# Optimization experiments

Hardware: AMD Instinct MI355X
Metric: run time of the kernel (lower is better)

Reference implementation:

```python
import jax, jax.numpy as jnp
import numpy as np

H, D, E, N, F = 16, 128, 2048, 2048, 8192
EPS = 1e-5


def setup_inputs() -> dict:
    key = jax.random.key(0)
    ks = jax.random.split(key, 11)
    u = lambda k, s: jax.random.uniform(k, s, dtype=jnp.float32)  # torch.rand init
    return {
        "token_embeddings": jax.random.normal(ks[0], (N, E), dtype=jnp.float32),
        "W_Q": u(ks[1], (H, E, D)),
        "W_K": u(ks[2], (H, E, D)),
        "W_V": u(ks[3], (H, E, D)),
        "W_Pool": u(ks[4], (H * D, E)),
        "W_1": u(ks[5], (E, F)),
        "b_1": u(ks[6], (1, F)),
        "W_2": u(ks[7], (F, E)),
        "b_2": u(ks[8], (1, E)),
        "gamma": u(ks[9], (1, 1)),
        "beta": u(ks[10], (1, E)),
    }


def _layer_norm(x, gamma, beta):
    mean = jnp.mean(x, axis=-1, keepdims=True)
    var = jnp.var(x, axis=-1, keepdims=True)  # unbiased=False
    return gamma * (x - mean) * jax.lax.rsqrt(var + EPS) + beta


def _mha(x, W_Q, W_K, W_V, W_Pool):
    # Q,K,V: [H, N, D]
    Q = jnp.einsum("ne,hed->hnd", x, W_Q)
    K = jnp.einsum("ne,hed->hnd", x, W_K)
    V = jnp.einsum("ne,hed->hnd", x, W_V)
    scores = jnp.einsum("hnd,hmd->hnm", Q, K) / jnp.sqrt(jnp.float32(D))
    causal = jnp.tril(jnp.ones((N, N), dtype=bool))
    scores = jnp.where(causal, scores, -jnp.inf)
    attn = jax.nn.softmax(scores, axis=-1)  # [H, N, N]
    heads = jnp.einsum("hnm,hmd->hnd", attn, V)  # [H, N, D]
    concat = jnp.transpose(heads, (1, 0, 2)).reshape(N, H * D)
    return concat @ W_Pool


def reference(token_embeddings, W_Q, W_K, W_V, W_Pool, W_1, b_1, W_2, b_2, gamma, beta):
    x = token_embeddings
    x = x + _mha(x, W_Q, W_K, W_V, W_Pool)
    x = _layer_norm(x, gamma, beta)
    ffn = jax.nn.relu(x @ W_1 + b_1) @ W_2 + b_2
    x = x + ffn
    x = _layer_norm(x, gamma, beta)
    return x
```

## Files before the change

kernel.cpp:

```cpp
#include <hip/hip_runtime.h>

typedef unsigned short u16;
typedef unsigned int   u32;
typedef __attribute__((ext_vector_type(4))) float f32x4;
typedef __attribute__((ext_vector_type(8))) short bf16x8;

#define MFMA_B16(a,b,c) __builtin_amdgcn_mfma_f32_16x16x32_bf16((a),(b),(c),0,0,0)

__device__ __forceinline__ u16 f2bf(float f){
  u32 u = __builtin_bit_cast(u32, f);
  u32 r = (u + 0x7FFFu + ((u >> 16) & 1u)) >> 16;
  return (u16)r;
}
__device__ __forceinline__ float bf2f(u16 h){
  u32 u = ((u32)h) << 16;
  return __builtin_bit_cast(float, u);
}
__device__ __forceinline__ void gload16(const void* g, void* l){
  __builtin_amdgcn_global_load_lds((const __attribute__((address_space(1))) void*)g,
                                   (__attribute__((address_space(3))) void*)l, 16, 0, 0);
}

__global__ __launch_bounds__(256) void pack_x2(const float* __restrict__ x,
                                               u16* __restrict__ xh, u16* __restrict__ xl){
  const int i = blockIdx.x*256 + threadIdx.x;
  const float v = x[i];
  const u16 hi = f2bf(v);
  xh[i] = hi;
  xl[i] = f2bf(v - bf2f(hi));
}

__global__ __launch_bounds__(256) void pack_qkv2(const float* __restrict__ WQ, const float* __restrict__ WK,
                                                 const float* __restrict__ WV,
                                                 u16* __restrict__ outh, u16* __restrict__ outl){
  __shared__ float t32[32][33];
  const int tid = threadIdx.x;
  const int tx = tid & 31, ty = tid >> 5;
  const int et = blockIdx.x >> 2, dt = blockIdx.x & 3;
  const int hh = blockIdx.y, tt = blockIdx.z;
  const float* W = (tt == 0 ? WQ : (tt == 1 ? WK : WV)) + (size_t)hh*2048*128;
  #pragma unroll
  for (int i = 0; i < 4; i++)
    t32[ty + i*8][tx] = W[(size_t)(et*32 + ty + i*8)*128 + dt*32 + tx];
  __syncthreads();
  const int j0 = tt*2048 + hh*128 + dt*32;
  #pragma unroll
  for (int i = 0; i < 4; i++){
    const float v = t32[tx][ty + i*8];
    const u16 hi = f2bf(v);
    const u16 lo = f2bf(v - bf2f(hi));
    const size_t idx = (size_t)(j0 + ty + i*8)*2048 + (et*32 + tx);
    outh[idx] = hi; outl[idx] = lo;
  }
}

__global__ __launch_bounds__(256) void tpack2(const float* __restrict__ in,
                                              u16* __restrict__ outh, u16* __restrict__ outl,
                                              int R, int C){
  __shared__ float t32[32][33];
  const int tid = threadIdx.x;
  const int tx = tid & 31, ty = tid >> 5;
  const int c0 = blockIdx.x*32, r0 = blockIdx.y*32;
  #pragma unroll
  for (int i = 0; i < 4; i++)
    t32[ty + i*8][tx] = in[(size_t)(r0 + ty + i*8)*C + c0 + tx];
  __syncthreads();
  #pragma unroll
  for (int i = 0; i < 4; i++){
    const float v = t32[tx][ty + i*8];
    const u16 hi = f2bf(v);
    const u16 lo = f2bf(v - bf2f(hi));
    const size_t idx = (size_t)(c0 + ty + i*8)*R + r0 + tx;
    outh[idx] = hi; outl[idx] = lo;
  }
}

template<int NS, int EPI, int SK>
__global__ __launch_bounds__(512, 2) void gemm8(
    const u16* __restrict__ Ah, const u16* __restrict__ Al,
    const u16* __restrict__ Bh, const u16* __restrict__ Bl,
    float* __restrict__ outf, u16* __restrict__ outb,
    const float* __restrict__ bias,
    u16* __restrict__ qh, u16* __restrict__ ql,
    u16* __restrict__ kh, u16* __restrict__ kl,
    u16* __restrict__ vTh, float* __restrict__ part,
    int M, int N, int K)
{
  __shared__ u16 LS[2][2][16384];
  const int tid = threadIdx.x;
  const int lane = tid & 63;
  const int w = tid >> 6;
  const int wr = w >> 2, wc = w & 3;
  const int l15 = lane & 15, lh = lane >> 4;
  const int nbx = N >> 8;
  int bsw = ((int)blockIdx.x & 7) * ((int)gridDim.x >> 3) + ((int)blockIdx.x >> 3);
  int slice = 0;
  if (SK == 4){ slice = bsw & 3; bsw >>= 2; }
  const int bx = bsw % nbx, by = bsw / nbx;
  const int m0 = by << 8, n0 = bx << 8;

  const int tiles_total = (NS * K) >> 6;
  const int nt = (SK == 4) ? (tiles_total >> 2) : tiles_total;
  const int t0 = (SK == 4) ? slice * nt : 0;

  auto stage = [&](int buf, int t){
    const int k0v = t << 6;
    const u16* Ap; const u16* Bp; int kk;
    if (NS == 1){ Ap = Ah; Bp = Bh; kk = k0v; }
    else if (NS == 2){
      if (k0v < K){ Ap = Ah; Bp = Bh; kk = k0v; }
      else        { Ap = Ah; Bp = Bl; kk = k0v - K; }
    } else {
      if (k0v < K)        { Ap = Ah; Bp = Bh; kk = k0v; }
      else if (k0v < 2*K) { Ap = Ah; Bp = Bl; kk = k0v - K; }
      else                { Ap = Al; Bp = Bh; kk = k0v - 2*K; }
    }
    u16* La = &LS[buf][0][0];
    u16* Lb = &LS[buf][1][0];
    #pragma unroll
    for (int q = 0; q < 4; q++){
      int s = q*512 + tid;
      int row = s >> 3, cc = (s & 7) ^ (row & 7);
      gload16(Ap + (size_t)(m0+row)*K + kk + cc*8, La + (q*512 + (tid & 448))*8);
    }
    #pragma unroll
    for (int q = 0; q < 4; q++){
      int s = q*512 + tid;
      int row = s >> 3, cc = (s & 7) ^ (row & 7);
      gload16(Bp + (size_t)(n0+row)*K + kk + cc*8, Lb + (q*512 + (tid & 448))*8);
    }
  };

  f32x4 acc[8][4] = {};
  bf16x8 bfr[4][2];

  stage(0, t0);
  for (int lt = 0; lt < nt; ++lt){
    const int buf = lt & 1;
    if (lt + 1 < nt){
      stage(buf ^ 1, t0 + lt + 1);
      asm volatile("s_waitcnt vmcnt(8)" ::: "memory");
    } else {
      asm volatile("s_waitcnt vmcnt(0)" ::: "memory");
    }
    asm volatile("" ::: "memory");
    __builtin_amdgcn_s_barrier();
    asm volatile("" ::: "memory");

    const u16* La = &LS[buf][0][0];
    const u16* Lb = &LS[buf][1][0];
    #pragma unroll
    for (int n = 0; n < 4; n++){
      int br = wc*64 + n*16 + l15;
      #pragma unroll
      for (int kt = 0; kt < 2; kt++){
        int c = (kt*4 + lh) ^ (br & 7);
        bfr[n][kt] = *(const bf16x8*)(Lb + br*64 + c*8);
      }
    }
    #pragma unroll
    for (int p = 0; p < 4; p++){
      if (p){
        asm volatile("" ::: "memory");
        __builtin_amdgcn_s_barrier();
        asm volatile("" ::: "memory");
      }
      bf16x8 af[2][2];
      #pragma unroll
      for (int i = 0; i < 2; i++){
        int ar = wr*128 + (2*p+i)*16 + l15;
        #pragma unroll
        for (int kt = 0; kt < 2; kt++){
          int c = (kt*4 + lh) ^ (ar & 7);
          af[i][kt] = *(const bf16x8*)(La + ar*64 + c*8);
        }
      }
      asm volatile("s_waitcnt lgkmcnt(0)" ::: "memory");
      __builtin_amdgcn_sched_barrier(0);
      __builtin_amdgcn_s_setprio(1);
      #pragma unroll
      for (int i = 0; i < 2; i++)
        #pragma unroll
        for (int n = 0; n < 4; n++)
          #pragma unroll
          for (int kt = 0; kt < 2; kt++)
            acc[2*p+i][n] = MFMA_B16(af[i][kt], bfr[n][kt], acc[2*p+i][n]);
      __builtin_amdgcn_s_setprio(0);
    }
    asm volatile("" ::: "memory");
    __builtin_amdgcn_s_barrier();
    asm volatile("" ::: "memory");
  }

  #pragma unroll
  for (int m = 0; m < 8; m++){
    #pragma unroll
    for (int n = 0; n < 4; n++){
      const int rbase = m0 + wr*128 + m*16 + lh*4;
      const int col = n0 + wc*64 + n*16 + l15;
      if (EPI == 0){
        const int plane = col >> 11;
        const int cj = col & 2047;
        if (plane == 2){
          ushort4 h4 = make_ushort4(f2bf(acc[m][n][0]), f2bf(acc[m][n][1]),
                                    f2bf(acc[m][n][2]), f2bf(acc[m][n][3]));
          *(ushort4*)(vTh + (size_t)cj*2048 + rbase) = h4;
        } else {
          u16* hp = (plane == 0) ? qh : kh;
          u16* lp = (plane == 0) ? ql : kl;
          #pragma unroll
          for (int r = 0; r < 4; r++){
            float v = acc[m][n][r];
            u16 hi = f2bf(v);
            u16 lo = f2bf(v - bf2f(hi));
            hp[(size_t)(rbase+r)*2048 + cj] = hi;
            lp[(size_t)(rbase+r)*2048 + cj] = lo;
          }
        }
      } else if (EPI == 2){
        const float b = bias[col];
        #pragma unroll
        for (int r = 0; r < 4; r++){
          float v = acc[m][n][r] + b;
          outb[(size_t)(rbase+r)*N + col] = f2bf(v > 0.f ? v : 0.f);
        }
      } else {
        float* dst = (slice < 3) ? (part + (size_t)slice*M*N) : outf;
        #pragma unroll
        for (int r = 0; r < 4; r++)
          dst[(size_t)(rbase+r)*N + col] = acc[m][n][r];
      }
    }
  }
}

__global__ __launch_bounds__(256) void ffn2_reduce(
    float* __restrict__ PR, const float* __restrict__ part,
    const float* __restrict__ H1, const float* __restrict__ b2)
{
  const size_t i4 = (size_t)blockIdx.x*256 + threadIdx.x;
  const size_t base = i4*4;
  const int col = (int)(base & 2047);
  float4 a  = ((float4*)PR)[i4];
  float4 p0 = ((const float4*)part)[i4];
  float4 p1 = ((const float4*)(part + 4194304))[i4];
  float4 p2 = ((const float4*)(part + 8388608))[i4];
  float4 h  = ((const float4*)H1)[i4];
  float4 b  = *(const float4*)(b2 + col);
  a.x = a.x + p0.x + p1.x + p2.x + h.x + b.x;
  a.y = a.y + p0.y + p1.y + p2.y + h.y + b.y;
  a.z = a.z + p0.z + p1.z + p2.z + h.z + b.z;
  a.w = a.w + p0.w + p1.w + p2.w + h.w + b.w;
  ((float4*)PR)[i4] = a;
}

__global__ __launch_bounds__(256) void gemm_bt(
    const u16* __restrict__ Ah, const u16* __restrict__ Bh,
    float* __restrict__ outf, const float* __restrict__ res,
    int M, int N, int K)
{
  __shared__ u16 As[2][128*64];
  __shared__ u16 Bs[2][128*64];
  const int tid = threadIdx.x;
  const int lane = tid & 63;
  const int w = tid >> 6;
  const int l15 = lane & 15, lh = lane >> 4;
  const int nbx = N >> 7;
  const int bsw = ((int)blockIdx.x & 7)*((int)gridDim.x >> 3) + ((int)blockIdx.x >> 3);
  const int bx = bsw % nbx, by = bsw / nbx;
  const int m0 = by << 7, n0 = bx << 7;
  const int wm = (w >> 1) << 6, wn = (w & 1) << 6;

  f32x4 acc[4][4] = {};
  const int NT = K >> 6;

  auto stage = [&](int buf, int kk){
    u16* Asb = &As[buf][0];
    u16* Bsb = &Bs[buf][0];
    #pragma unroll
    for (int q = 0; q < 4; q++){
      int s = q*256 + tid;
      int row = s >> 3, cc = (s & 7) ^ (row & 7);
      gload16(Ah + (size_t)(m0+row)*K + kk + cc*8, Asb + (q*256 + (tid & 192))*8);
    }
    #pragma unroll
    for (int q = 0; q < 4; q++){
      int s = q*256 + tid;
      int row = s >> 3, cc = (s & 7) ^ (row & 7);
      gload16(Bh + (size_t)(n0+row)*K + kk + cc*8, Bsb + (q*256 + (tid & 192))*8);
    }
  };

  stage(0, 0);
  for (int t = 0; t < NT; ++t){
    const int cur = t & 1;
    if (t + 1 < NT){
      stage(cur ^ 1, (t + 1) << 6);
      asm volatile("s_waitcnt vmcnt(8)" ::: "memory");
    } else {
      asm volatile("s_waitcnt vmcnt(0)" ::: "memory");
    }
    __builtin_amdgcn_s_barrier();
    asm volatile("" ::: "memory");

    const u16* Asb = &As[cur][0];
    const u16* Bsb = &Bs[cur][0];
    #pragma unroll
    for (int kt = 0; kt < 2; kt++){
      bf16x8 af[4], bfr[4];
      #pragma unroll
      for (int m = 0; m < 4; m++){
        int row = wm + m*16 + l15;
        int c = (kt*4 + lh) ^ (row & 7);
        af[m] = *(const bf16x8*)(Asb + row*64 + c*8);
      }
      #pragma unroll
      for (int n = 0; n < 4; n++){
        int row = wn + n*16 + l15;
        int c = (kt*4 + lh) ^ (row & 7);
        bfr[n] = *(const bf16x8*)(Bsb + row*64 + c*8);
      }
      #pragma unroll
      for (int m = 0; m < 4; m++)
        #pragma unroll
        for (int n = 0; n < 4; n++)
          acc[m][n] = MFMA_B16(af[m], bfr[n], acc[m][n]);
    }
    asm volatile("" ::: "memory");
    __builtin_amdgcn_s_barrier();
    asm volatile("" ::: "memory");
  }

  #pragma unroll
  for (int m = 0; m < 4; m++){
    #pragma unroll
    for (int n = 0; n < 4; n++){
      const int rbase = m0 + wm + m*16 + lh*4;
      const int col = n0 + wn + n*16 + l15;
      #pragma unroll
      for (int r = 0; r < 4; r++){
        size_t idx = (size_t)(rbase+r)*N + col;
        outf[idx] = acc[m][n][r] + res[idx];
      }
    }
  }
}

__global__ __launch_bounds__(256) void attn_k(
    const u16* __restrict__ qh, const u16* __restrict__ ql,
    const u16* __restrict__ kh, const u16* __restrict__ kl,
    const u16* __restrict__ vT, u16* __restrict__ atth)
{
  __shared__ u16 Khs[64*128];
  __shared__ u16 Kls[64*128];
  __shared__ u16 Vhs[128*64];
  __shared__ u16 Phs[4*16*64];

  const int tid = threadIdx.x;
  const int lane = tid & 63;
  const int w = tid >> 6;
  const int l15 = lane & 15, lh = lane >> 4;
  const int h = blockIdx.y;
  const int qb = blockIdx.x;
  const int qbase = qb << 6;
  const float scale = 0.088388347648318447f;

  bf16x8 qfh[4], qfl[4];
  {
    const int qrow = qbase + w*16 + l15;
    const u16* ph = qh + (size_t)qrow*2048 + h*128 + lh*8;
    const u16* pl = ql + (size_t)qrow*2048 + h*128 + lh*8;
    #pragma unroll
    for (int kt = 0; kt < 4; kt++){
      qfh[kt] = *(const bf16x8*)(ph + kt*32);
      qfl[kt] = *(const bf16x8*)(pl + kt*32);
    }
  }

  f32x4 acco[8] = {};
  float mrun[4] = {-1e30f,-1e30f,-1e30f,-1e30f};
  float lrun[4] = {0.f,0.f,0.f,0.f};
  const int qrow0 = qbase + w*16 + lh*4;
  u16* pwh = Phs + w*1024;

  const int nkv = qb + 1;
  for (int kvt = 0; kvt < nkv; kvt++){
    const int kv0 = kvt << 6;
    __syncthreads();
    #pragma unroll
    for (int q = 0; q < 4; q++){
      int s = q*256 + tid;
      int row = s >> 4, c = (s & 15) ^ (row & 7);
      gload16(kh + (size_t)(kv0+row)*2048 + h*128 + c*8, Khs + (q*256 + (tid & 192))*8);
    }
    #pragma unroll
    for (int q = 0; q < 4; q++){
      int s = q*256 + tid;
      int row = s >> 4, c = (s & 15) ^ (row & 7);
      gload16(kl + (size_t)(kv0+row)*2048 + h*128 + c*8, Kls + (q*256 + (tid & 192))*8);
    }
    #pragma unroll
    for (int q = 0; q < 4; q++){
      int s = q*256 + tid;
      int d = s >> 3, c = (s & 7) ^ (d & 7);
      gload16(vT + (size_t)(h*128+d)*2048 + kv0 + c*8, Vhs + (q*256 + (tid & 192))*8);
    }
    asm volatile("s_waitcnt vmcnt(0)" ::: "memory");
    __syncthreads();

    f32x4 sac[4] = {};
    __builtin_amdgcn_s_setprio(1);
    #pragma unroll
    for (int n = 0; n < 4; n++){
      const int kvr = n*16 + l15;
      const u16* kb  = Khs + kvr*128;
      const u16* klb = Kls + kvr*128;
      const int sw = kvr & 7;
      #pragma unroll
      for (int kt = 0; kt < 4; kt++){
        const int c = (kt*4 + lh) ^ sw;
        bf16x8 bh = *(const bf16x8*)(kb + c*8);
        bf16x8 bl = *(const bf16x8*)(klb + c*8);
        sac[n] = MFMA_B16(qfh[kt], bh, sac[n]);
        sac[n] = MFMA_B16(qfh[kt], bl, sac[n]);
        sac[n] = MFMA_B16(qfl[kt], bh, sac[n]);
      }
    }
    __builtin_amdgcn_s_setprio(0);

    float p[4][4];
    float tm[4] = {-1e30f,-1e30f,-1e30f,-1e30f};
    #pragma unroll
    for (int n = 0; n < 4; n++){
      const int kvg = kv0 + n*16 + l15;
      #pragma unroll
      for (int r = 0; r < 4; r++){
        float s = sac[n][r] * scale;
        if (kvg > qrow0 + r) s = -1e30f;
        p[n][r] = s;
        tm[r] = fmaxf(tm[r], s);
      }
    }
    #pragma unroll
    for (int r = 0; r < 4; r++){
      tm[r] = fmaxf(tm[r], __shfl_xor(tm[r], 1));
      tm[r] = fmaxf(tm[r], __shfl_xor(tm[r], 2));
      tm[r] = fmaxf(tm[r], __shfl_xor(tm[r], 4));
      tm[r] = fmaxf(tm[r], __shfl_xor(tm[r], 8));
    }
    float corr[4];
    #pragma unroll
    for (int r = 0; r < 4; r++){
      float mn = fmaxf(mrun[r], tm[r]);
      corr[r] = __expf(mrun[r] - mn);
      mrun[r] = mn;
    }
    #pragma unroll
    for (int r = 0; r < 4; r++){
      float sum = 0.f;
      #pragma unroll
      for (int n = 0; n < 4; n++){
        float pv = __expf(p[n][r] - mrun[r]);
        p[n][r] = pv;
        sum += pv;
      }
      sum += __shfl_xor(sum, 1);
      sum += __shfl_xor(sum, 2);
      sum += __shfl_xor(sum, 4);
      sum += __shfl_xor(sum, 8);
      lrun[r] = lrun[r]*corr[r] + sum;
    }
    #pragma unroll
    for (int nn = 0; nn < 8; nn++)
      #pragma unroll
      for (int r = 0; r < 4; r++)
        acco[nn][r] *= corr[r];

    #pragma unroll
    for (int n = 0; n < 4; n++){
      const int colb = n*16 + l15;
      #pragma unroll
      for (int r = 0; r < 4; r++){
        const int row = lh*4 + r;
        const int off = row*64 + (((colb>>3) ^ (row&7))<<3) + (colb&7);
        pwh[off] = f2bf(p[n][r]);
      }
    }
    asm volatile("" ::: "memory");

    __builtin_amdgcn_s_setprio(1);
    #pragma unroll
    for (int kt2 = 0; kt2 < 2; kt2++){
      const int ac = (kt2*4 + lh) ^ (l15 & 7);
      bf16x8 afh = *(const bf16x8*)(pwh + l15*64 + ac*8);
      #pragma unroll
      for (int n = 0; n < 8; n++){
        const int d = n*16 + l15;
        const int c = (kt2*4 + lh) ^ (d & 7);
        bf16x8 bvh = *(const bf16x8*)(Vhs + d*64 + c*8);
        acco[n] = MFMA_B16(afh, bvh, acco[n]);
      }
    }
    __builtin_amdgcn_s_setprio(0);
  }

  #pragma unroll
  for (int n = 0; n < 8; n++){
    const int col = h*128 + n*16 + l15;
    #pragma unroll
    for (int r = 0; r < 4; r++){
      atth[(size_t)(qrow0+r)*2048 + col] = f2bf(acco[n][r] / lrun[r]);
    }
  }
}

template<int WSPLIT>
__global__ __launch_bounds__(256) void ln_k(
    const float* __restrict__ in, float* __restrict__ outf,
    u16* __restrict__ outh, u16* __restrict__ outl,
    const float* __restrict__ gptr, const float* __restrict__ beta)
{
  const int tid = threadIdx.x;
  const int lane = tid & 63;
  const int w = tid >> 6;
  const int row = blockIdx.x;
  const float4* xr = (const float4*)(in + (size_t)row*2048);
  float4 a = xr[tid];
  float4 b = xr[tid + 256];
  float s = a.x+a.y+a.z+a.w + b.x+b.y+b.z+b.w;
  #pragma unroll
  for (int off = 32; off; off >>= 1) s += __shfl_xor(s, off);
  __shared__ float red[8];
  if (lane == 0) red[w] = s;
  __syncthreads();
  const float mean = (red[0]+red[1]+red[2]+red[3]) * (1.0f/2048.0f);
  float q =
    (a.x-mean)*(a.x-mean) + (a.y-mean)*(a.y-mean) + (a.z-mean)*(a.z-mean) + (a.w-mean)*(a.w-mean) +
    (b.x-mean)*(b.x-mean) + (b.y-mean)*(b.y-mean) + (b.z-mean)*(b.z-mean) + (b.w-mean)*(b.w-mean);
  #pragma unroll
  for (int off = 32; off; off >>= 1) q += __shfl_xor(q, off);
  if (lane == 0) red[4 + w] = q;
  __syncthreads();
  const float var = (red[4]+red[5]+red[6]+red[7]) * (1.0f/2048.0f);
  const float sc = rsqrtf(var + 1e-5f) * gptr[0];
  const float4 be0 = ((const float4*)beta)[tid];
  const float4 be1 = ((const float4*)beta)[tid + 256];
  float4 o0, o1;
  o0.x = (a.x-mean)*sc + be0.x; o0.y = (a.y-mean)*sc + be0.y;
  o0.z = (a.z-mean)*sc + be0.z; o0.w = (a.w-mean)*sc + be0.w;
  o1.x = (b.x-mean)*sc + be1.x; o1.y = (b.y-mean)*sc + be1.y;
  o1.z = (b.z-mean)*sc + be1.z; o1.w = (b.w-mean)*sc + be1.w;
  float4* orow = (float4*)(outf + (size_t)row*2048);
  orow[tid] = o0; orow[tid+256] = o1;
  if (WSPLIT){
    ushort4 h0 = make_ushort4(f2bf(o0.x), f2bf(o0.y), f2bf(o0.z), f2bf(o0.w));
    ushort4 h1 = make_ushort4(f2bf(o1.x), f2bf(o1.y), f2bf(o1.z), f2bf(o1.w));
    ushort4* hrow = (ushort4*)(outh + (size_t)row*2048);
    hrow[tid] = h0; hrow[tid+256] = h1;
    if (outl){
      ushort4 L0 = make_ushort4(f2bf(o0.x - bf2f(h0.x)), f2bf(o0.y - bf2f(h0.y)),
                                f2bf(o0.z - bf2f(h0.z)), f2bf(o0.w - bf2f(h0.w)));
      ushort4 L1 = make_ushort4(f2bf(o1.x - bf2f(h1.x)), f2bf(o1.y - bf2f(h1.y)),
                                f2bf(o1.z - bf2f(h1.z)), f2bf(o1.w - bf2f(h1.w)));
      ushort4* lrow = (ushort4*)(outl + (size_t)row*2048);
      lrow[tid] = L0; lrow[tid+256] = L1;
    }
  }
}

extern "C" void kernel_launch(void* const* d_in, const int* in_sizes, int n_in,
                              void* d_out, int out_size, void* d_ws, size_t ws_size,
                              hipStream_t stream)
{
  const float* x   = (const float*)d_in[0];
  const float* WQ  = (const float*)d_in[1];
  const float* WK  = (const float*)d_in[2];
  const float* WV  = (const float*)d_in[3];
  const float* WP  = (const float*)d_in[4];
  const float* W1  = (const float*)d_in[5];
  const float* b1  = (const float*)d_in[6];
  const float* W2  = (const float*)d_in[7];
  const float* b2  = (const float*)d_in[8];
  const float* gam = (const float*)d_in[9];
  const float* bet = (const float*)d_in[10];
  float* out = (float*)d_out;
  (void)in_sizes; (void)n_in; (void)out_size; (void)ws_size;

  const size_t NP = 2048ull*2048;
  char* pR1 = (char*)d_ws;
  char* pR2 = pR1 + (64ull<<20);
  char* pR3 = pR2 + (32ull<<20);
  char* pR4 = pR3 + (48ull<<20);
  char* pR5 = pR4 + (16ull<<20);

  u16* Wh   = (u16*)pR1;
  u16* Wl   = (u16*)(pR1 + (32ull<<20));
  u16* xh   = (u16*)pR2;
  u16* xl   = xh + NP;
  u16* a1   = (u16*)pR2;
  u16* qh_  = (u16*)pR3;
  u16* ql_  = qh_ + NP;
  u16* kh_  = ql_ + NP;
  u16* kl_  = kh_ + NP;
  u16* vT_  = kl_ + NP;
  u16* Hh   = (u16*)pR3;
  float* part = (float*)pR3;
  u16* ATTh = (u16*)pR4;
  float* H1 = (float*)pR4;
  float* PR = (float*)pR5;

  pack_x2 <<<2048*2048/256, 256, 0, stream>>>(x, xh, xl);
  pack_qkv2<<<dim3(256,16,3), 256, 0, stream>>>(WQ, WK, WV, Wh, Wl);
  gemm8<3,0,1><<<192, 512, 0, stream>>>(xh, xl, Wh, Wl, nullptr, nullptr, nullptr,
                                        qh_, ql_, kh_, kl_, vT_, nullptr, 2048, 6144, 2048);
  attn_k<<<dim3(32,16), 256, 0, stream>>>(qh_, ql_, kh_, kl_, vT_, ATTh);
  tpack2<<<dim3(64,64), 256, 0, stream>>>(WP, Wh, Wl, 2048, 2048);
  gemm_bt<<<256, 256, 0, stream>>>(ATTh, Wh, PR, x, 2048, 2048, 2048);
  ln_k<1><<<2048, 256, 0, stream>>>(PR, H1, Hh, nullptr, gam, bet);
  tpack2<<<dim3(256,64), 256, 0, stream>>>(W1, Wh, Wl, 2048, 8192);
  gemm8<1,2,1><<<256, 512, 0, stream>>>(Hh, nullptr, Wh, nullptr, nullptr, a1, b1,
                                        nullptr, nullptr, nullptr, nullptr, nullptr, nullptr,
                                        2048, 8192, 2048);
  tpack2<<<dim3(64,256), 256, 0, stream>>>(W2, Wh, Wl, 8192, 2048);
  gemm8<2,4,4><<<256, 512, 0, stream>>>(a1, nullptr, Wh, Wl, PR, nullptr, nullptr,
                                        nullptr, nullptr, nullptr, nullptr, nullptr, part,
                                        2048, 2048, 8192);
  ffn2_reduce<<<4096, 256, 0, stream>>>(PR, part, H1, b2);
  ln_k<0><<<2048, 256, 0, stream>>>(PR, out, nullptr, nullptr, gam, bet);
}
```

Before: 643.3 us.

## Retile QKV GEMM to 256x192, fuse FFN2 reduce into final layernorm, skip unused lo writes

Templates gemm8 on the number of column fragments per wave so the QKV projection uses 256x192 tiles, giving 256 blocks instead of 192 for a fuller fill of the CUs. The split-K partial reduction for FFN2 is fused into the final layernorm kernel, removing one launch and a full read and write of the intermediate. tpack2 gains a flag so the lo-half weight planes are written only where a GEMM consumes them, and ln_k drops its unused template path. The new tile shape leaves LDS use and the waitcnt counts per tile different from the tuned 256x256 path.

```diff
diff --git a/kernel.cpp b/kernel.cpp
--- a/kernel.cpp
+++ b/kernel.cpp
@@ -54,6 +54,7 @@
   }
 }
 
+template<int WLO>
 __global__ __launch_bounds__(256) void tpack2(const float* __restrict__ in,
                                               u16* __restrict__ outh, u16* __restrict__ outl,
                                               int R, int C){
@@ -69,13 +70,13 @@
   for (int i = 0; i < 4; i++){
     const float v = t32[tx][ty + i*8];
     const u16 hi = f2bf(v);
-    const u16 lo = f2bf(v - bf2f(hi));
     const size_t idx = (size_t)(c0 + ty + i*8)*R + r0 + tx;
-    outh[idx] = hi; outl[idx] = lo;
-  }
-}
-
-template<int NS, int EPI, int SK>
+    outh[idx] = hi;
+    if (WLO) outl[idx] = f2bf(v - bf2f(hi));
+  }
+}
+
+template<int NS, int EPI, int SK, int NWC>
 __global__ __launch_bounds__(512, 2) void gemm8(
     const u16* __restrict__ Ah, const u16* __restrict__ Al,
     const u16* __restrict__ Bh, const u16* __restrict__ Bl,
@@ -86,18 +87,20 @@
     u16* __restrict__ vTh, float* __restrict__ part,
     int M, int N, int K)
 {
-  __shared__ u16 LS[2][2][16384];
+  constexpr int BN = 64 * NWC;
+  __shared__ u16 LA[2][256*64];
+  __shared__ u16 LB[2][BN*64];
   const int tid = threadIdx.x;
   const int lane = tid & 63;
   const int w = tid >> 6;
   const int wr = w >> 2, wc = w & 3;
   const int l15 = lane & 15, lh = lane >> 4;
-  const int nbx = N >> 8;
+  const int nbx = N / BN;
   int bsw = ((int)blockIdx.x & 7) * ((int)gridDim.x >> 3) + ((int)blockIdx.x >> 3);
   int slice = 0;
   if (SK == 4){ slice = bsw & 3; bsw >>= 2; }
   const int bx = bsw % nbx, by = bsw / nbx;
-  const int m0 = by << 8, n0 = bx << 8;
+  const int m0 = by << 8, n0 = bx * BN;
 
   const int tiles_total = (NS * K) >> 6;
   const int nt = (SK == 4) ? (tiles_total >> 2) : tiles_total;
@@ -115,8 +118,8 @@
       else if (k0v < 2*K) { Ap = Ah; Bp = Bl; kk = k0v - K; }
       else                { Ap = Al; Bp = Bh; kk = k0v - 2*K; }
     }
-    u16* La = &LS[buf][0][0];
-    u16* Lb = &LS[buf][1][0];
+    u16* La = &LA[buf][0];
+    u16* Lb = &LB[buf][0];
     #pragma unroll
     for (int q = 0; q < 4; q++){
       int s = q*512 + tid;
@@ -124,22 +127,23 @@
       gload16(Ap + (size_t)(m0+row)*K + kk + cc*8, La + (q*512 + (tid & 448))*8);
     }
     #pragma unroll
-    for (int q = 0; q < 4; q++){
+    for (int q = 0; q < NWC; q++){
       int s = q*512 + tid;
       int row = s >> 3, cc = (s & 7) ^ (row & 7);
       gload16(Bp + (size_t)(n0+row)*K + kk + cc*8, Lb + (q*512 + (tid & 448))*8);
     }
   };
 
-  f32x4 acc[8][4] = {};
-  bf16x8 bfr[4][2];
+  f32x4 acc[8][NWC] = {};
+  bf16x8 bfr[NWC][2];
 
   stage(0, t0);
   for (int lt = 0; lt < nt; ++lt){
     const int buf = lt & 1;
     if (lt + 1 < nt){
       stage(buf ^ 1, t0 + lt + 1);
-      asm volatile("s_waitcnt vmcnt(8)" ::: "memory");
+      if constexpr (NWC == 3) asm volatile("s_waitcnt vmcnt(7)" ::: "memory");
+      else                    asm volatile("s_waitcnt vmcnt(8)" ::: "memory");
     } else {
       asm volatile("s_waitcnt vmcnt(0)" ::: "memory");
     }
@@ -147,11 +151,11 @@
     __builtin_amdgcn_s_barrier();
     asm volatile("" ::: "memory");
 
-    const u16* La = &LS[buf][0][0];
-    const u16* Lb = &LS[buf][1][0];
-    #pragma unroll
-    for (int n = 0; n < 4; n++){
-      int br = wc*64 + n*16 + l15;
+    const u16* La = &LA[buf][0];
+    const u16* Lb = &LB[buf][0];
+    #pragma unroll
+    for (int n = 0; n < NWC; n++){
+      int br = wc*(16*NWC) + n*16 + l15;
       #pragma unroll
       for (int kt = 0; kt < 2; kt++){
         int c = (kt*4 + lh) ^ (br & 7);
@@ -181,7 +185,7 @@
       #pragma unroll
       for (int i = 0; i < 2; i++)
         #pragma unroll
-        for (int n = 0; n < 4; n++)
+        for (int n = 0; n < NWC; n++)
           #pragma unroll
           for (int kt = 0; kt < 2; kt++)
             acc[2*p+i][n] = MFMA_B16(af[i][kt], bfr[n][kt], acc[2*p+i][n]);
@@ -195,9 +199,9 @@
   #pragma unroll
   for (int m = 0; m < 8; m++){
     #pragma unroll
-    for (int n = 0; n < 4; n++){
+    for (int n = 0; n < NWC; n++){
       const int rbase = m0 + wr*128 + m*16 + lh*4;
-      const int col = n0 + wc*64 + n*16 + l15;
+      const int col = n0 + wc*(16*NWC) + n*16 + l15;
       if (EPI == 0){
         const int plane = col >> 11;
         const int cj = col & 2047;
@@ -234,24 +238,56 @@
   }
 }
 
-__global__ __launch_bounds__(256) void ffn2_reduce(
-    float* __restrict__ PR, const float* __restrict__ part,
-    const float* __restrict__ H1, const float* __restrict__ b2)
+__global__ __launch_bounds__(256) void ln2_fused(
+    const float* __restrict__ p3, const float* __restrict__ part,
+    const float* __restrict__ H1, const float* __restrict__ b2,
+    float* __restrict__ outf, const float* __restrict__ gptr,
+    const float* __restrict__ beta)
 {
-  const size_t i4 = (size_t)blockIdx.x*256 + threadIdx.x;
-  const size_t base = i4*4;
-  const int col = (int)(base & 2047);
-  float4 a  = ((float4*)PR)[i4];
-  float4 p0 = ((const float4*)part)[i4];
-  float4 p1 = ((const float4*)(part + 4194304))[i4];
-  float4 p2 = ((const float4*)(part + 8388608))[i4];
-  float4 h  = ((const float4*)H1)[i4];
-  float4 b  = *(const float4*)(b2 + col);
-  a.x = a.x + p0.x + p1.x + p2.x + h.x + b.x;
-  a.y = a.y + p0.y + p1.y + p2.y + h.y + b.y;
-  a.z = a.z + p0.z + p1.z + p2.z + h.z + b.z;
-  a.w = a.w + p0.w + p1.w + p2.w + h.w + b.w;
-  ((float4*)PR)[i4] = a;
+  const int tid = threadIdx.x;
+  const int lane = tid & 63;
+  const int w = tid >> 6;
+  const int row = blockIdx.x;
+  const size_t ro = (size_t)row * 2048;
+  const size_t NP = 4194304;
+  auto ld = [&](const float* p, int t){ return ((const float4*)(p + ro))[t]; };
+  float4 a  = ld(p3, tid),        c  = ld(p3, tid + 256);
+  float4 a0 = ld(part, tid),      c0 = ld(part, tid + 256);
+  float4 a1 = ld(part+NP, tid),   c1 = ld(part+NP, tid + 256);
+  float4 a2 = ld(part+2*NP, tid), c2 = ld(part+2*NP, tid + 256);
+  float4 ah = ld(H1, tid),        ch = ld(H1, tid + 256);
+  float4 ab = ((const float4*)b2)[tid];
+  float4 cb = ((const float4*)b2)[tid + 256];
+  a.x += a0.x + a1.x + a2.x + ah.x + ab.x;  a.y += a0.y + a1.y + a2.y + ah.y + ab.y;
+  a.z += a0.z + a1.z + a2.z + ah.z + ab.z;  a.w += a0.w + a1.w + a2.w + ah.w + ab.w;
+  c.x += c0.x + c1.x + c2.x + ch.x + cb.x;  c.y += c0.y + c1.y + c2.y + ch.y + cb.y;
+  c.z += c0.z + c1.z + c2.z + ch.z + cb.z;  c.w += c0.w + c1.w + c2.w + ch.w + cb.w;
+
+  float s = a.x+a.y+a.z+a.w + c.x+c.y+c.z+c.w;
+  #pragma unroll
+  for (int off = 32; off; off >>= 1) s += __shfl_xor(s, off);
+  __shared__ float red[8];
+  if (lane == 0) red[w] = s;
+  __syncthreads();
+  const float mean = (red[0]+red[1]+red[2]+red[3]) * (1.0f/2048.0f);
+  float q =
+    (a.x-mean)*(a.x-mean) + (a.y-mean)*(a.y-mean) + (a.z-mean)*(a.z-mean) + (a.w-mean)*(a.w-mean) +
+    (c.x-mean)*(c.x-mean) + (c.y-mean)*(c.y-mean) + (c.z-mean)*(c.z-mean) + (c.w-mean)*(c.w-mean);
+  #pragma unroll
+  for (int off = 32; off; off >>= 1) q += __shfl_xor(q, off);
+  if (lane == 0) red[4 + w] = q;
+  __syncthreads();
+  const float var = (red[4]+red[5]+red[6]+red[7]) * (1.0f/2048.0f);
+  const float sc = rsqrtf(var + 1e-5f) * gptr[0];
+  const float4 be0 = ((const float4*)beta)[tid];
+  const float4 be1 = ((const float4*)beta)[tid + 256];
+  float4 o0, o1;
+  o0.x = (a.x-mean)*sc + be0.x; o0.y = (a.y-mean)*sc + be0.y;
+  o0.z = (a.z-mean)*sc + be0.z; o0.w = (a.w-mean)*sc + be0.w;
+  o1.x = (c.x-mean)*sc + be1.x; o1.y = (c.y-mean)*sc + be1.y;
+  o1.z = (c.z-mean)*sc + be1.z; o1.w = (c.w-mean)*sc + be1.w;
+  float4* orow = (float4*)(outf + ro);
+  orow[tid] = o0; orow[tid+256] = o1;
 }
 
 __global__ __launch_bounds__(256) void gemm_bt(
@@ -514,10 +550,9 @@
   }
 }
 
-template<int WSPLIT>
 __global__ __launch_bounds__(256) void ln_k(
     const float* __restrict__ in, float* __restrict__ outf,
-    u16* __restrict__ outh, u16* __restrict__ outl,
+    u16* __restrict__ outh,
     const float* __restrict__ gptr, const float* __restrict__ beta)
 {
   const int tid = threadIdx.x;
@@ -552,20 +587,10 @@
   o1.z = (b.z-mean)*sc + be1.z; o1.w = (b.w-mean)*sc + be1.w;
   float4* orow = (float4*)(outf + (size_t)row*2048);
   orow[tid] = o0; orow[tid+256] = o1;
-  if (WSPLIT){
-    ushort4 h0 = make_ushort4(f2bf(o0.x), f2bf(o0.y), f2bf(o0.z), f2bf(o0.w));
-    ushort4 h1 = make_ushort4(f2bf(o1.x), f2bf(o1.y), f2bf(o1.z), f2bf(o1.w));
-    ushort4* hrow = (ushort4*)(outh + (size_t)row*2048);
-    hrow[tid] = h0; hrow[tid+256] = h1;
-    if (outl){
-      ushort4 L0 = make_ushort4(f2bf(o0.x - bf2f(h0.x)), f2bf(o0.y - bf2f(h0.y)),
-                                f2bf(o0.z - bf2f(h0.z)), f2bf(o0.w - bf2f(h0.w)));
-      ushort4 L1 = make_ushort4(f2bf(o1.x - bf2f(h1.x)), f2bf(o1.y - bf2f(h1.y)),
-                                f2bf(o1.z - bf2f(h1.z)), f2bf(o1.w - bf2f(h1.w)));
-      ushort4* lrow = (ushort4*)(outl + (size_t)row*2048);
-      lrow[tid] = L0; lrow[tid+256] = L1;
-    }
-  }
+  ushort4 h0 = make_ushort4(f2bf(o0.x), f2bf(o0.y), f2bf(o0.z), f2bf(o0.w));
+  ushort4 h1 = make_ushort4(f2bf(o1.x), f2bf(o1.y), f2bf(o1.z), f2bf(o1.w));
+  ushort4* hrow = (ushort4*)(outh + (size_t)row*2048);
+  hrow[tid] = h0; hrow[tid+256] = h1;
 }
 
 extern "C" void kernel_launch(void* const* d_in, const int* in_sizes, int n_in,
@@ -611,20 +636,19 @@
 
   pack_x2 <<<2048*2048/256, 256, 0, stream>>>(x, xh, xl);
   pack_qkv2<<<dim3(256,16,3), 256, 0, stream>>>(WQ, WK, WV, Wh, Wl);
-  gemm8<3,0,1><<<192, 512, 0, stream>>>(xh, xl, Wh, Wl, nullptr, nullptr, nullptr,
-                                        qh_, ql_, kh_, kl_, vT_, nullptr, 2048, 6144, 2048);
+  gemm8<3,0,1,3><<<256, 512, 0, stream>>>(xh, xl, Wh, Wl, nullptr, nullptr, nullptr,
+                                          qh_, ql_, kh_, kl_, vT_, nullptr, 2048, 6144, 2048);
   attn_k<<<dim3(32,16), 256, 0, stream>>>(qh_, ql_, kh_, kl_, vT_, ATTh);
-  tpack2<<<dim3(64,64), 256, 0, stream>>>(WP, Wh, Wl, 2048, 2048);
+  tpack2<0><<<dim3(64,64), 256, 0, stream>>>(WP, Wh, nullptr, 2048, 2048);
   gemm_bt<<<256, 256, 0, stream>>>(ATTh, Wh, PR, x, 2048, 2048, 2048);
-  ln_k<1><<<2048, 256, 0, stream>>>(PR, H1, Hh, nullptr, gam, bet);
-  tpack2<<<dim3(256,64), 256, 0, stream>>>(W1, Wh, Wl, 2048, 8192);
-  gemm8<1,2,1><<<256, 512, 0, stream>>>(Hh, nullptr, Wh, nullptr, nullptr, a1, b1,
-                                        nullptr, nullptr, nullptr, nullptr, nullptr, nullptr,
-                                        2048, 8192, 2048);
-  tpack2<<<dim3(64,256), 256, 0, stream>>>(W2, Wh, Wl, 8192, 2048);
-  gemm8<2,4,4><<<256, 512, 0, stream>>>(a1, nullptr, Wh, Wl, PR, nullptr, nullptr,
-                                        nullptr, nullptr, nullptr, nullptr, nullptr, part,
-                                        2048, 2048, 8192);
-  ffn2_reduce<<<4096, 256, 0, stream>>>(PR, part, H1, b2);
-  ln_k<0><<<2048, 256, 0, stream>>>(PR, out, nullptr, nullptr, gam, bet);
-}
+  ln_k<<<2048, 256, 0, stream>>>(PR, H1, Hh, gam, bet);
+  tpack2<0><<<dim3(256,64), 256, 0, stream>>>(W1, Wh, nullptr, 2048, 8192);
+  gemm8<1,2,1,4><<<256, 512, 0, stream>>>(Hh, nullptr, Wh, nullptr, nullptr, a1, b1,
+                                          nullptr, nullptr, nullptr, nullptr, nullptr, nullptr,
+                                          2048, 8192, 2048);
+  tpack2<1><<<dim3(64,256), 256, 0, stream>>>(W2, Wh, Wl, 8192, 2048);
+  gemm8<2,4,4,4><<<256, 512, 0, stream>>>(a1, nullptr, Wh, Wl, PR, nullptr, nullptr,
+                                          nullptr, nullptr, nullptr, nullptr, nullptr, part,
+                                          2048, 2048, 8192);
+  ln2_fused<<<2048, 256, 0, stream>>>(PR, part, H1, b2, out, gam, bet);
+}
```

New measurement: 682.0 us. +6.0%, slower.
